# Kernel tuning notes

Hardware: AMD Instinct MI355X
Metric: run time of the kernel (lower is better)

## Reference

```python
import jax, jax.numpy as jnp
import numpy as np

D_MODEL = 1024
D_KEY = 64
N_HEADS = 16
B, T = 4, 2048


def setup_inputs() -> dict:
    key = jax.random.key(0)
    ks = jax.random.split(key, 12)
    s = 0.02
    return {
        "keys": jax.random.normal(ks[0], (B, T, D_MODEL), jnp.float32),
        "queries": jax.random.normal(ks[1], (B, T, D_MODEL), jnp.float32),
        "values": jax.random.normal(ks[2], (B, T, D_MODEL), jnp.float32),
        "pad_mask": jnp.ones((B, T), jnp.int32),
        "WK_w": jax.random.normal(ks[3], (D_KEY * N_HEADS, D_MODEL), jnp.float32) * s,
        "WK_b": jnp.zeros((D_KEY * N_HEADS,), jnp.float32),
        "WQ_w": jax.random.normal(ks[4], (D_KEY * N_HEADS, D_MODEL), jnp.float32) * s,
        "WQ_b": jnp.zeros((D_KEY * N_HEADS,), jnp.float32),
        "WV_w": jax.random.normal(ks[5], (D_KEY * N_HEADS, D_MODEL), jnp.float32) * s,
        "WV_b": jnp.zeros((D_KEY * N_HEADS,), jnp.float32),
        "WO_w": jax.random.normal(ks[6], (D_MODEL, D_KEY * N_HEADS), jnp.float32) * s,
        "WO_b": jnp.zeros((D_MODEL,), jnp.float32),
    }


def reference(keys, queries, values, pad_mask, WK_w, WK_b, WQ_w, WQ_b, WV_w, WV_b, WO_w, WO_b):
    # NOTE: the original torch module calls masked_fill (non-inplace) and discards
    # the result, so neither the causal mask nor pad_mask has any effect. We
    # faithfully reproduce that: no masking. pad_mask is an unused constant.
    batch, time = keys.shape[:2]
    k = keys @ WK_w.T + WK_b      # [B,T,H*dk]
    q = queries @ WQ_w.T + WQ_b
    v = values @ WV_w.T + WV_b

    def split_heads(x):
        return x.reshape(batch, time, N_HEADS, D_KEY).transpose(0, 2, 1, 3)  # [B,H,T,dk]

    k, q, v = split_heads(k), split_heads(q), split_heads(v)
    # scores[t,s] = k_t . q_s / sqrt(d_key)  (K and Q swapped, as in source)
    scores = jnp.einsum("bhtd,bhsd->bhts", k, q) / jnp.sqrt(jnp.float32(D_KEY))
    attn = jax.nn.softmax(scores, axis=-1)             # [B,H,T,T]
    ctx = jnp.einsum("bhts,bhsd->bhtd", attn, v)       # [B,H,T,dk]
    ctx = ctx.transpose(0, 2, 1, 3).reshape(batch, time, N_HEADS * D_KEY)
    return ctx @ WO_w.T + WO_b
```

## Files before the change

### kernel.cpp

```cpp
#include <hip/hip_runtime.h>

typedef unsigned short u16;
typedef unsigned int u32;
typedef __attribute__((ext_vector_type(8))) short short8;
typedef __attribute__((ext_vector_type(4))) float f32x4;

__device__ __forceinline__ u16 f2bf(float f) {
    unsigned int u = __float_as_uint(f);
    u += 0x7fffu + ((u >> 16) & 1u);
    return (u16)(u >> 16);
}

__device__ __forceinline__ u32 pack_trunc(float a, float b) {
    return __builtin_amdgcn_perm(__float_as_uint(b), __float_as_uint(a), 0x07060302u);
}

__device__ __forceinline__ void gload16(const u16* g, const u16* l) {
    __builtin_amdgcn_global_load_lds(
        (const __attribute__((address_space(1))) unsigned int*)g,
        (__attribute__((address_space(3))) unsigned int*)l, 16, 0, 0);
}

__global__ __launch_bounds__(256) void cast_all(const float* __restrict__ k,
                                                const float* __restrict__ q,
                                                const float* __restrict__ v,
                                                const float* __restrict__ wk,
                                                const float* __restrict__ wq,
                                                const float* __restrict__ wv,
                                                const float* __restrict__ wo,
                                                u16* __restrict__ Xk, u16* __restrict__ Xq,
                                                u16* __restrict__ Xv, u16* __restrict__ Wk,
                                                u16* __restrict__ Wq, u16* __restrict__ Wv,
                                                u16* __restrict__ Wo) {
    size_t i = ((size_t)blockIdx.x * 256 + threadIdx.x) * 8;
    const float* src; u16* dst; size_t off;
    if (i < 25165824) {
        int r = (int)(i >> 23); off = i & 8388607;
        src = r == 0 ? k : (r == 1 ? q : v);
        dst = r == 0 ? Xk : (r == 1 ? Xq : Xv);
    } else {
        size_t j = i - 25165824;
        int r = (int)(j >> 20); off = j & 1048575;
        src = r == 0 ? wk : (r == 1 ? wq : (r == 2 ? wv : wo));
        dst = r == 0 ? Wk : (r == 1 ? Wq : (r == 2 ? Wv : Wo));
    }
    float4 a = *(const float4*)(src + off);
    float4 b = *(const float4*)(src + off + 4);
    union { u16 h[8]; uint4 u; } r8;
    r8.h[0] = f2bf(a.x); r8.h[1] = f2bf(a.y); r8.h[2] = f2bf(a.z); r8.h[3] = f2bf(a.w);
    r8.h[4] = f2bf(b.x); r8.h[5] = f2bf(b.y); r8.h[6] = f2bf(b.z); r8.h[7] = f2bf(b.w);
    *(uint4*)(dst + off) = r8.u;
}

__global__ __launch_bounds__(256) void gemm_qkv(const u16* __restrict__ Xk,
                                                const u16* __restrict__ Xq,
                                                const u16* __restrict__ Xv,
                                                const u16* __restrict__ Wk,
                                                const u16* __restrict__ Wq,
                                                const u16* __restrict__ Wv,
                                                const float* __restrict__ bK,
                                                const float* __restrict__ bQ,
                                                const float* __restrict__ bV,
                                                u16* __restrict__ Kbh,
                                                u16* __restrict__ Qbh,
                                                u16* __restrict__ Vtg,
                                                float kscale) {
    __shared__ u16 sA[128 * 32];
    __shared__ u16 sB[128 * 32];
    const int f = blockIdx.x;
    const int z = f >> 9;
    const int r9 = f & 511;
    const int i_idx = (r9 & 7) | (((r9 >> 6) & 7) << 3);
    const int j_idx = (r9 >> 3) & 7;

    const u16* X = z == 0 ? Xk : (z == 1 ? Xq : Xv);
    const u16* W = z == 0 ? Wk : (z == 1 ? Wq : Wv);
    const float* bias = z == 0 ? bK : (z == 1 ? bQ : bV);
    u16* out = z == 0 ? Kbh : (z == 1 ? Qbh : Vtg);
    const float scale = z == 0 ? kscale : 1.0f;

    const int tid  = threadIdx.x;
    const int wave = tid >> 6, lane = tid & 63;
    const int quad = lane >> 4, l16 = lane & 15;
    const int wm = wave & 1, wn = wave >> 1;
    const int i0 = i_idx * 128, j0 = j_idx * 128;
    const int lrow = tid >> 2, lseg = tid & 3;

    f32x4 acc[4][4];
    #pragma unroll
    for (int mt = 0; mt < 4; mt++)
        #pragma unroll
        for (int nt = 0; nt < 4; nt++) acc[mt][nt] = (f32x4){0.f, 0.f, 0.f, 0.f};

    const u16* gA0 = X + (size_t)(i0 + lrow) * 1024 + lseg * 8;
    const u16* gA1 = X + (size_t)(i0 + 64 + lrow) * 1024 + lseg * 8;
    const u16* gB0 = W + (size_t)(j0 + lrow) * 1024 + lseg * 8;
    const u16* gB1 = W + (size_t)(j0 + 64 + lrow) * 1024 + lseg * 8;
    const u16* lA0 = sA + wave * 512;
    const u16* lA1 = sA + 2048 + wave * 512;
    const u16* lB0 = sB + wave * 512;
    const u16* lB1 = sB + 2048 + wave * 512;

    for (int kk = 0; kk < 1024; kk += 32) {
        __syncthreads();
        gload16(gA0 + kk, lA0);
        gload16(gA1 + kk, lA1);
        gload16(gB0 + kk, lB0);
        gload16(gB1 + kk, lB1);
        __syncthreads();
        short8 af[4], bf[4];
        #pragma unroll
        for (int mt = 0; mt < 4; mt++)
            af[mt] = *(const short8*)&sA[(wm * 64 + mt * 16 + l16) * 32 + quad * 8];
        #pragma unroll
        for (int nt = 0; nt < 4; nt++)
            bf[nt] = *(const short8*)&sB[(wn * 64 + nt * 16 + l16) * 32 + quad * 8];
        #pragma unroll
        for (int mt = 0; mt < 4; mt++)
            #pragma unroll
            for (int nt = 0; nt < 4; nt++)
                acc[mt][nt] = __builtin_amdgcn_mfma_f32_16x16x32_bf16(af[mt], bf[nt], acc[mt][nt], 0, 0, 0);
    }

    #pragma unroll
    for (int mt = 0; mt < 4; mt++) {
        #pragma unroll
        for (int nt = 0; nt < 4; nt++) {
            int j = j0 + wn * 64 + nt * 16 + l16;
            float bj = bias[j];
            #pragma unroll
            for (int r = 0; r < 4; r++) {
                int i = i0 + wm * 64 + mt * 16 + quad * 4 + r;
                float v = (acc[mt][nt][r] + bj) * scale;
                int b = i >> 11, t = i & 2047;
                int h = j >> 6,  dd = j & 63;
                size_t idx;
                if (z == 2) idx = (((size_t)(b * 16 + h)) * 64 + dd) * 2048 + t;
                else        idx = (((size_t)(b * 16 + h)) * 2048 + t) * 64 + dd;
                out[idx] = f2bf(v);
            }
        }
    }
}

__global__ __launch_bounds__(256) void gemm_out(const u16* __restrict__ X,
                                                const u16* __restrict__ W,
                                                const float* __restrict__ bias,
                                                float* __restrict__ out) {
    __shared__ u16 sA[128 * 32];
    __shared__ u16 sB[64 * 32];
    const int f = blockIdx.x;
    const int j_idx = (f >> 3) & 15;
    const int i_idx = (f & 7) | ((f >> 7) << 3);
    const int tid  = threadIdx.x;
    const int wave = tid >> 6, lane = tid & 63;
    const int quad = lane >> 4, l16 = lane & 15;
    const int wm = wave & 1, wn = wave >> 1;
    const int i0 = i_idx * 128, j0 = j_idx * 64;
    const int lrow = tid >> 2, lseg = tid & 3;

    f32x4 acc[4][2];
    #pragma unroll
    for (int mt = 0; mt < 4; mt++) {
        acc[mt][0] = (f32x4){0.f, 0.f, 0.f, 0.f};
        acc[mt][1] = (f32x4){0.f, 0.f, 0.f, 0.f};
    }

    const u16* gA0 = X + (size_t)(i0 + lrow) * 1024 + lseg * 8;
    const u16* gA1 = X + (size_t)(i0 + 64 + lrow) * 1024 + lseg * 8;
    const u16* gB0 = W + (size_t)(j0 + lrow) * 1024 + lseg * 8;
    const u16* lA0 = sA + wave * 512;
    const u16* lA1 = sA + 2048 + wave * 512;
    const u16* lB0 = sB + wave * 512;

    for (int kk = 0; kk < 1024; kk += 32) {
        __syncthreads();
        gload16(gA0 + kk, lA0);
        gload16(gA1 + kk, lA1);
        gload16(gB0 + kk, lB0);
        __syncthreads();
        short8 af[4], bf[2];
        #pragma unroll
        for (int mt = 0; mt < 4; mt++)
            af[mt] = *(const short8*)&sA[(wm * 64 + mt * 16 + l16) * 32 + quad * 8];
        #pragma unroll
        for (int nt = 0; nt < 2; nt++)
            bf[nt] = *(const short8*)&sB[(wn * 32 + nt * 16 + l16) * 32 + quad * 8];
        #pragma unroll
        for (int mt = 0; mt < 4; mt++)
            #pragma unroll
            for (int nt = 0; nt < 2; nt++)
                acc[mt][nt] = __builtin_amdgcn_mfma_f32_16x16x32_bf16(af[mt], bf[nt], acc[mt][nt], 0, 0, 0);
    }

    #pragma unroll
    for (int mt = 0; mt < 4; mt++) {
        #pragma unroll
        for (int nt = 0; nt < 2; nt++) {
            int j = j0 + wn * 32 + nt * 16 + l16;
            float bj = bias[j];
            #pragma unroll
            for (int r = 0; r < 4; r++) {
                int i = i0 + wm * 64 + mt * 16 + quad * 4 + r;
                out[(size_t)i * 1024 + j] = acc[mt][nt][r] + bj;
            }
        }
    }
}

#define QST 72

__global__ __launch_bounds__(256, 2) void attn_kernel(const u16* __restrict__ Kbh,
                                                      const u16* __restrict__ Qbh,
                                                      const u16* __restrict__ Vtg,
                                                      u16* __restrict__ ctx) {
    __shared__ u16 sQ[64 * QST];
    __shared__ u16 sVt[64 * QST];
    __shared__ u16 sP[4 * 2 * 16 * QST];
    const int f = blockIdx.x;
    const int bh = (f & 7) | ((f >> 6) << 3);
    const int tx = (f >> 3) & 7;
    const int tid  = threadIdx.x;
    const int wave = tid >> 6, lane = tid & 63;
    const int quad = lane >> 4, l16 = lane & 15;
    const int t0 = tx * 256;
    const int tw = t0 + wave * 64;
    const size_t base = (size_t)bh * 2048 * 64;

    short8 bk[4][2];
    #pragma unroll
    for (int g = 0; g < 4; g++) {
        const u16* kr = Kbh + base + (size_t)(tw + g * 16 + l16) * 64 + quad * 8;
        bk[g][0] = *(const short8*)kr;
        bk[g][1] = *(const short8*)(kr + 32);
    }
    const short8 ones = {0x3F80, 0x3F80, 0x3F80, 0x3F80, 0x3F80, 0x3F80, 0x3F80, 0x3F80};

    f32x4 accO[4][4];
    #pragma unroll
    for (int g = 0; g < 4; g++)
        #pragma unroll
        for (int dt = 0; dt < 4; dt++) accO[g][dt] = (f32x4){0.f, 0.f, 0.f, 0.f};
    f32x4 accL[4];
    #pragma unroll
    for (int g = 0; g < 4; g++) accL[g] = (f32x4){0.f, 0.f, 0.f, 0.f};

    const int srow = tid >> 2, seg = tid & 3;
    u16* sPw = sP + wave * 2 * 16 * QST;

    for (int s0 = 0; s0 < 2048; s0 += 64) {
        __syncthreads();
        {
            const uint4* gq = (const uint4*)(Qbh + base + (size_t)(s0 + srow) * 64 + seg * 16);
            uint4 q0 = gq[0], q1 = gq[1];
            *(uint4*)&sQ[srow * QST + seg * 16]     = q0;
            *(uint4*)&sQ[srow * QST + seg * 16 + 8] = q1;
        }
        {
            const uint4* gv = (const uint4*)(Vtg + ((size_t)bh * 64 + srow) * 2048 + s0 + seg * 16);
            uint4 v0 = gv[0], v1 = gv[1];
            *(uint4*)&sVt[srow * QST + seg * 16]     = v0;
            *(uint4*)&sVt[srow * QST + seg * 16 + 8] = v1;
        }
        __syncthreads();

        short8 aq[4][2], av[2][4];
        #pragma unroll
        for (int nt = 0; nt < 4; nt++) {
            aq[nt][0] = *(const short8*)&sQ[(nt * 16 + l16) * QST + quad * 8];
            aq[nt][1] = *(const short8*)&sQ[(nt * 16 + l16) * QST + 32 + quad * 8];
        }
        #pragma unroll
        for (int kk = 0; kk < 2; kk++)
            #pragma unroll
            for (int dt = 0; dt < 4; dt++)
                av[kk][dt] = *(const short8*)&sVt[(dt * 16 + l16) * QST + kk * 32 + quad * 8];

        #pragma unroll
        for (int g = 0; g < 4; g++) {
            f32x4 aS[4];
            #pragma unroll
            for (int nt = 0; nt < 4; nt++) {
                f32x4 s = __builtin_amdgcn_mfma_f32_16x16x32_bf16(aq[nt][0], bk[g][0],
                            (f32x4){0.f, 0.f, 0.f, 0.f}, 0, 0, 0);
                aS[nt] = __builtin_amdgcn_mfma_f32_16x16x32_bf16(aq[nt][1], bk[g][1], s, 0, 0, 0);
            }
            u16* pb = sPw + (g & 1) * 16 * QST;
            #pragma unroll
            for (int nt = 0; nt < 4; nt++) {
                float p0 = __builtin_amdgcn_exp2f(aS[nt][0]);
                float p1 = __builtin_amdgcn_exp2f(aS[nt][1]);
                float p2 = __builtin_amdgcn_exp2f(aS[nt][2]);
                float p3 = __builtin_amdgcn_exp2f(aS[nt][3]);
                uint2 pk = { pack_trunc(p0, p1), pack_trunc(p2, p3) };
                *(uint2*)&pb[l16 * QST + nt * 16 + quad * 4] = pk;
            }
            #pragma unroll
            for (int kk = 0; kk < 2; kk++) {
                short8 bp = *(const short8*)&pb[l16 * QST + kk * 32 + quad * 8];
                accL[g] = __builtin_amdgcn_mfma_f32_16x16x32_bf16(ones, bp, accL[g], 0, 0, 0);
                #pragma unroll
                for (int dt = 0; dt < 4; dt++)
                    accO[g][dt] = __builtin_amdgcn_mfma_f32_16x16x32_bf16(av[kk][dt], bp, accO[g][dt], 0, 0, 0);
            }
        }
    }

    const int b = bh >> 4, h = bh & 15;
    #pragma unroll
    for (int g = 0; g < 4; g++) {
        float inv = 1.f / accL[g][0];
        int t = tw + g * 16 + l16;
        u16* orow = ctx + ((size_t)(b * 2048 + t)) * 1024 + h * 64;
        #pragma unroll
        for (int dt = 0; dt < 4; dt++) {
            union { u16 h4[4]; uint2 u; } o;
            #pragma unroll
            for (int r = 0; r < 4; r++) o.h4[r] = f2bf(accO[g][dt][r] * inv);
            *(uint2*)&orow[dt * 16 + quad * 4] = o.u;
        }
    }
}

extern "C" void kernel_launch(void* const* d_in, const int* in_sizes, int n_in,
                              void* d_out, int out_size, void* d_ws, size_t ws_size,
                              hipStream_t stream) {
    const float* keys    = (const float*)d_in[0];
    const float* queries = (const float*)d_in[1];
    const float* values  = (const float*)d_in[2];
    const float* WKb = (const float*)d_in[5];
    const float* WQb = (const float*)d_in[7];
    const float* WVb = (const float*)d_in[9];
    const float* WOb = (const float*)d_in[11];

    char* ws = (char*)d_ws;
    const size_t MB = 1 << 20;
    u16* Kbh = (u16*)(ws + 0 * MB);
    u16* Qbh = (u16*)(ws + 16 * MB);
    u16* Vtg = (u16*)(ws + 32 * MB);
    u16* Xk  = (u16*)(ws + 48 * MB);
    u16* Xq  = (u16*)(ws + 64 * MB);
    u16* Xv  = (u16*)(ws + 80 * MB);
    u16* Wk  = (u16*)(ws + 96 * MB);
    u16* Wq  = (u16*)(ws + 98 * MB);
    u16* Wv  = (u16*)(ws + 100 * MB);
    u16* Wo  = (u16*)(ws + 102 * MB);
    u16* ctx = (u16*)(ws + 48 * MB);

    cast_all<<<14336, 256, 0, stream>>>(keys, queries, values,
                                        (const float*)d_in[4], (const float*)d_in[6],
                                        (const float*)d_in[8], (const float*)d_in[10],
                                        Xk, Xq, Xv, Wk, Wq, Wv, Wo);

    const float kscale = 1.4426950408889634f * 0.125f;
    gemm_qkv<<<1536, 256, 0, stream>>>(Xk, Xq, Xv, Wk, Wq, Wv,
                                       WKb, WQb, WVb, Kbh, Qbh, Vtg, kscale);

    attn_kernel<<<512, 256, 0, stream>>>(Kbh, Qbh, Vtg, ctx);

    gemm_out<<<1024, 256, 0, stream>>>(ctx, Wo, WOb, (float*)d_out);
}
```

Before: 346.0 us.

## Fuse fp32-to-bf16 casts into GEMM tile loads and drop the cast kernel

Result: slower. 441.9 us (+27.7%).

```diff
diff --git a/kernel.cpp b/kernel.cpp
--- a/kernel.cpp
+++ b/kernel.cpp
@@ -15,66 +15,31 @@
     return __builtin_amdgcn_perm(__float_as_uint(b), __float_as_uint(a), 0x07060302u);
 }
 
-__device__ __forceinline__ void gload16(const u16* g, const u16* l) {
-    __builtin_amdgcn_global_load_lds(
-        (const __attribute__((address_space(1))) unsigned int*)g,
-        (__attribute__((address_space(3))) unsigned int*)l, 16, 0, 0);
-}
-
-__global__ __launch_bounds__(256) void cast_all(const float* __restrict__ k,
-                                                const float* __restrict__ q,
-                                                const float* __restrict__ v,
-                                                const float* __restrict__ wk,
-                                                const float* __restrict__ wq,
-                                                const float* __restrict__ wv,
-                                                const float* __restrict__ wo,
-                                                u16* __restrict__ Xk, u16* __restrict__ Xq,
-                                                u16* __restrict__ Xv, u16* __restrict__ Wk,
-                                                u16* __restrict__ Wq, u16* __restrict__ Wv,
-                                                u16* __restrict__ Wo) {
-    size_t i = ((size_t)blockIdx.x * 256 + threadIdx.x) * 8;
-    const float* src; u16* dst; size_t off;
-    if (i < 25165824) {
-        int r = (int)(i >> 23); off = i & 8388607;
-        src = r == 0 ? k : (r == 1 ? q : v);
-        dst = r == 0 ? Xk : (r == 1 ? Xq : Xv);
-    } else {
-        size_t j = i - 25165824;
-        int r = (int)(j >> 20); off = j & 1048575;
-        src = r == 0 ? wk : (r == 1 ? wq : (r == 2 ? wv : wo));
-        dst = r == 0 ? Wk : (r == 1 ? Wq : (r == 2 ? Wv : Wo));
-    }
-    float4 a = *(const float4*)(src + off);
-    float4 b = *(const float4*)(src + off + 4);
-    union { u16 h[8]; uint4 u; } r8;
-    r8.h[0] = f2bf(a.x); r8.h[1] = f2bf(a.y); r8.h[2] = f2bf(a.z); r8.h[3] = f2bf(a.w);
-    r8.h[4] = f2bf(b.x); r8.h[5] = f2bf(b.y); r8.h[6] = f2bf(b.z); r8.h[7] = f2bf(b.w);
-    *(uint4*)(dst + off) = r8.u;
-}
-
-__global__ __launch_bounds__(256) void gemm_qkv(const u16* __restrict__ Xk,
-                                                const u16* __restrict__ Xq,
-                                                const u16* __restrict__ Xv,
-                                                const u16* __restrict__ Wk,
-                                                const u16* __restrict__ Wq,
-                                                const u16* __restrict__ Wv,
-                                                const float* __restrict__ bK,
-                                                const float* __restrict__ bQ,
-                                                const float* __restrict__ bV,
-                                                u16* __restrict__ Kbh,
-                                                u16* __restrict__ Qbh,
-                                                u16* __restrict__ Vtg,
-                                                float kscale) {
-    __shared__ u16 sA[128 * 32];
-    __shared__ u16 sB[128 * 32];
+#define AST 72
+
+__global__ __launch_bounds__(256, 3) void gemm_qkv(const float* __restrict__ Xk,
+                                                   const float* __restrict__ Xq,
+                                                   const float* __restrict__ Xv,
+                                                   const float* __restrict__ Wk,
+                                                   const float* __restrict__ Wq,
+                                                   const float* __restrict__ Wv,
+                                                   const float* __restrict__ bK,
+                                                   const float* __restrict__ bQ,
+                                                   const float* __restrict__ bV,
+                                                   u16* __restrict__ Kbh,
+                                                   u16* __restrict__ Qbh,
+                                                   u16* __restrict__ Vtg,
+                                                   float kscale) {
+    __shared__ u16 sA[128 * AST];
+    __shared__ u16 sB[128 * AST];
     const int f = blockIdx.x;
     const int z = f >> 9;
     const int r9 = f & 511;
     const int i_idx = (r9 & 7) | (((r9 >> 6) & 7) << 3);
     const int j_idx = (r9 >> 3) & 7;
 
-    const u16* X = z == 0 ? Xk : (z == 1 ? Xq : Xv);
-    const u16* W = z == 0 ? Wk : (z == 1 ? Wq : Wv);
+    const float* X = z == 0 ? Xk : (z == 1 ? Xq : Xv);
+    const float* W = z == 0 ? Wk : (z == 1 ? Wq : Wv);
     const float* bias = z == 0 ? bK : (z == 1 ? bQ : bV);
     u16* out = z == 0 ? Kbh : (z == 1 ? Qbh : Vtg);
     const float scale = z == 0 ? kscale : 1.0f;
@@ -84,7 +49,7 @@
     const int quad = lane >> 4, l16 = lane & 15;
     const int wm = wave & 1, wn = wave >> 1;
     const int i0 = i_idx * 128, j0 = j_idx * 128;
-    const int lrow = tid >> 2, lseg = tid & 3;
+    const int srow = tid >> 3, sseg = tid & 7;
 
     f32x4 acc[4][4];
     #pragma unroll
@@ -92,34 +57,44 @@
         #pragma unroll
         for (int nt = 0; nt < 4; nt++) acc[mt][nt] = (f32x4){0.f, 0.f, 0.f, 0.f};
 
-    const u16* gA0 = X + (size_t)(i0 + lrow) * 1024 + lseg * 8;
-    const u16* gA1 = X + (size_t)(i0 + 64 + lrow) * 1024 + lseg * 8;
-    const u16* gB0 = W + (size_t)(j0 + lrow) * 1024 + lseg * 8;
-    const u16* gB1 = W + (size_t)(j0 + 64 + lrow) * 1024 + lseg * 8;
-    const u16* lA0 = sA + wave * 512;
-    const u16* lA1 = sA + 2048 + wave * 512;
-    const u16* lB0 = sB + wave * 512;
-    const u16* lB1 = sB + 2048 + wave * 512;
-
-    for (int kk = 0; kk < 1024; kk += 32) {
-        __syncthreads();
-        gload16(gA0 + kk, lA0);
-        gload16(gA1 + kk, lA1);
-        gload16(gB0 + kk, lB0);
-        gload16(gB1 + kk, lB1);
-        __syncthreads();
-        short8 af[4], bf[4];
-        #pragma unroll
-        for (int mt = 0; mt < 4; mt++)
-            af[mt] = *(const short8*)&sA[(wm * 64 + mt * 16 + l16) * 32 + quad * 8];
-        #pragma unroll
-        for (int nt = 0; nt < 4; nt++)
-            bf[nt] = *(const short8*)&sB[(wn * 64 + nt * 16 + l16) * 32 + quad * 8];
-        #pragma unroll
-        for (int mt = 0; mt < 4; mt++)
+    for (int kk = 0; kk < 1024; kk += 64) {
+        __syncthreads();
+        #pragma unroll
+        for (int p = 0; p < 4; p++) {
+            int r = p * 32 + srow;
+            const float* g = X + (size_t)(i0 + r) * 1024 + kk + sseg * 8;
+            float4 v0 = *(const float4*)g;
+            float4 v1 = *(const float4*)(g + 4);
+            uint4 pk = { pack_trunc(v0.x, v0.y), pack_trunc(v0.z, v0.w),
+                         pack_trunc(v1.x, v1.y), pack_trunc(v1.z, v1.w) };
+            *(uint4*)&sA[r * AST + sseg * 8] = pk;
+        }
+        #pragma unroll
+        for (int p = 0; p < 4; p++) {
+            int r = p * 32 + srow;
+            const float* g = W + (size_t)(j0 + r) * 1024 + kk + sseg * 8;
+            float4 v0 = *(const float4*)g;
+            float4 v1 = *(const float4*)(g + 4);
+            uint4 pk = { pack_trunc(v0.x, v0.y), pack_trunc(v0.z, v0.w),
+                         pack_trunc(v1.x, v1.y), pack_trunc(v1.z, v1.w) };
+            *(uint4*)&sB[r * AST + sseg * 8] = pk;
+        }
+        __syncthreads();
+        #pragma unroll
+        for (int ks = 0; ks < 2; ks++) {
+            short8 af[4], bf[4];
+            #pragma unroll
+            for (int mt = 0; mt < 4; mt++)
+                af[mt] = *(const short8*)&sA[(wm * 64 + mt * 16 + l16) * AST + ks * 32 + quad * 8];
             #pragma unroll
             for (int nt = 0; nt < 4; nt++)
-                acc[mt][nt] = __builtin_amdgcn_mfma_f32_16x16x32_bf16(af[mt], bf[nt], acc[mt][nt], 0, 0, 0);
+                bf[nt] = *(const short8*)&sB[(wn * 64 + nt * 16 + l16) * AST + ks * 32 + quad * 8];
+            #pragma unroll
+            for (int mt = 0; mt < 4; mt++)
+                #pragma unroll
+                for (int nt = 0; nt < 4; nt++)
+                    acc[mt][nt] = __builtin_amdgcn_mfma_f32_16x16x32_bf16(af[mt], bf[nt], acc[mt][nt], 0, 0, 0);
+        }
     }
 
     #pragma unroll
@@ -143,12 +118,14 @@
     }
 }
 
+#define OST 40
+
 __global__ __launch_bounds__(256) void gemm_out(const u16* __restrict__ X,
-                                                const u16* __restrict__ W,
+                                                const float* __restrict__ W,
                                                 const float* __restrict__ bias,
                                                 float* __restrict__ out) {
-    __shared__ u16 sA[128 * 32];
-    __shared__ u16 sB[64 * 32];
+    __shared__ u16 sA[128 * OST];
+    __shared__ u16 sB[64 * OST];
     const int f = blockIdx.x;
     const int j_idx = (f >> 3) & 15;
     const int i_idx = (f & 7) | ((f >> 7) << 3);
@@ -157,7 +134,7 @@
     const int quad = lane >> 4, l16 = lane & 15;
     const int wm = wave & 1, wn = wave >> 1;
     const int i0 = i_idx * 128, j0 = j_idx * 64;
-    const int lrow = tid >> 2, lseg = tid & 3;
+    const int arow = tid >> 2, aseg = tid & 3;
 
     f32x4 acc[4][2];
     #pragma unroll
@@ -166,26 +143,30 @@
         acc[mt][1] = (f32x4){0.f, 0.f, 0.f, 0.f};
     }
 
-    const u16* gA0 = X + (size_t)(i0 + lrow) * 1024 + lseg * 8;
-    const u16* gA1 = X + (size_t)(i0 + 64 + lrow) * 1024 + lseg * 8;
-    const u16* gB0 = W + (size_t)(j0 + lrow) * 1024 + lseg * 8;
-    const u16* lA0 = sA + wave * 512;
-    const u16* lA1 = sA + 2048 + wave * 512;
-    const u16* lB0 = sB + wave * 512;
-
     for (int kk = 0; kk < 1024; kk += 32) {
         __syncthreads();
-        gload16(gA0 + kk, lA0);
-        gload16(gA1 + kk, lA1);
-        gload16(gB0 + kk, lB0);
+        #pragma unroll
+        for (int p = 0; p < 2; p++) {
+            int r = p * 64 + arow;
+            uint4 v = *(const uint4*)(X + (size_t)(i0 + r) * 1024 + kk + aseg * 8);
+            *(uint4*)&sA[r * OST + aseg * 8] = v;
+        }
+        {
+            const float* g = W + (size_t)(j0 + arow) * 1024 + kk + aseg * 8;
+            float4 v0 = *(const float4*)g;
+            float4 v1 = *(const float4*)(g + 4);
+            uint4 pk = { pack_trunc(v0.x, v0.y), pack_trunc(v0.z, v0.w),
+                         pack_trunc(v1.x, v1.y), pack_trunc(v1.z, v1.w) };
+            *(uint4*)&sB[arow * OST + aseg * 8] = pk;
+        }
         __syncthreads();
         short8 af[4], bf[2];
         #pragma unroll
         for (int mt = 0; mt < 4; mt++)
-            af[mt] = *(const short8*)&sA[(wm * 64 + mt * 16 + l16) * 32 + quad * 8];
+            af[mt] = *(const short8*)&sA[(wm * 64 + mt * 16 + l16) * OST + quad * 8];
         #pragma unroll
         for (int nt = 0; nt < 2; nt++)
-            bf[nt] = *(const short8*)&sB[(wn * 32 + nt * 16 + l16) * 32 + quad * 8];
+            bf[nt] = *(const short8*)&sB[(wn * 32 + nt * 16 + l16) * OST + quad * 8];
         #pragma unroll
         for (int mt = 0; mt < 4; mt++)
             #pragma unroll
@@ -328,9 +309,13 @@
     const float* keys    = (const float*)d_in[0];
     const float* queries = (const float*)d_in[1];
     const float* values  = (const float*)d_in[2];
+    const float* WKw = (const float*)d_in[4];
     const float* WKb = (const float*)d_in[5];
+    const float* WQw = (const float*)d_in[6];
     const float* WQb = (const float*)d_in[7];
+    const float* WVw = (const float*)d_in[8];
     const float* WVb = (const float*)d_in[9];
+    const float* WOw = (const float*)d_in[10];
     const float* WOb = (const float*)d_in[11];
 
     char* ws = (char*)d_ws;
@@ -338,25 +323,13 @@
     u16* Kbh = (u16*)(ws + 0 * MB);
     u16* Qbh = (u16*)(ws + 16 * MB);
     u16* Vtg = (u16*)(ws + 32 * MB);
-    u16* Xk  = (u16*)(ws + 48 * MB);
-    u16* Xq  = (u16*)(ws + 64 * MB);
-    u16* Xv  = (u16*)(ws + 80 * MB);
-    u16* Wk  = (u16*)(ws + 96 * MB);
-    u16* Wq  = (u16*)(ws + 98 * MB);
-    u16* Wv  = (u16*)(ws + 100 * MB);
-    u16* Wo  = (u16*)(ws + 102 * MB);
     u16* ctx = (u16*)(ws + 48 * MB);
 
-    cast_all<<<14336, 256, 0, stream>>>(keys, queries, values,
-                                        (const float*)d_in[4], (const float*)d_in[6],
-                                        (const float*)d_in[8], (const float*)d_in[10],
-                                        Xk, Xq, Xv, Wk, Wq, Wv, Wo);
-
     const float kscale = 1.4426950408889634f * 0.125f;
-    gemm_qkv<<<1536, 256, 0, stream>>>(Xk, Xq, Xv, Wk, Wq, Wv,
+    gemm_qkv<<<1536, 256, 0, stream>>>(keys, queries, values, WKw, WQw, WVw,
                                        WKb, WQb, WVb, Kbh, Qbh, Vtg, kscale);
 
     attn_kernel<<<512, 256, 0, stream>>>(Kbh, Qbh, Vtg, ctx);
 
-    gemm_out<<<1024, 256, 0, stream>>>(ctx, Wo, WOb, (float*)d_out);
-}
+    gemm_out<<<1024, 256, 0, stream>>>(ctx, WOw, WOb, (float*)d_out);
+}
```
